# Kernel tuning notes

Measured on AMD Instinct MI355X. Metric: run time of the kernel, lower is better.

The kernel has to match this reference:

```python
import jax, jax.numpy as jnp
import numpy as np

V = 100000   # input_size == output_size (item vocab)
H = 256      # hidden_size
B = 512      # batch_size
L = 1        # num_layers


def setup_inputs() -> dict:
    key = jax.random.key(0)
    k0, k1, k2, k3, k4 = jax.random.split(key, 5)
    s = 1.0 / np.sqrt(H)  # pytorch default uniform bound scale
    return {
        "input": jax.random.randint(k0, (B,), 0, V),
        "target": jax.random.randint(k1, (B,), 0, V),
        "hidden": jnp.zeros((L, B, H), jnp.float32),
        # GRU weights, pytorch gate layout [r; z; n]
        "w_ih": jax.random.uniform(k2, (3 * H, V), jnp.float32, -s, s),
        "w_hh": jax.random.uniform(k3, (3 * H, H), jnp.float32, -s, s),
        "b_ih": jnp.zeros((3 * H,), jnp.float32),
        "b_hh": jnp.zeros((3 * H,), jnp.float32),
        # h2o linear
        "w_out": jax.random.uniform(k4, (V, H), jnp.float32, -s, s),
        "b_out": jnp.zeros((V,), jnp.float32),
    }


def reference(input, target, hidden, w_ih, w_hh, b_ih, b_hh, w_out, b_out):
    # one-hot(input) @ w_ih.T is mathematically a column gather of w_ih
    h = hidden[0]                                        # (B, H)
    gi = jnp.take(w_ih, input, axis=1).T + b_ih          # (B, 3H)
    gh = h @ w_hh.T + b_hh                               # (B, 3H)
    i_r, i_z, i_n = jnp.split(gi, 3, axis=1)
    h_r, h_z, h_n = jnp.split(gh, 3, axis=1)
    r = jax.nn.sigmoid(i_r + h_r)
    z = jax.nn.sigmoid(i_z + h_z)
    n = jnp.tanh(i_n + r * h_n)
    h_new = (1.0 - z) * n + z * h                        # (B, H)
    logit = jnp.tanh(h_new @ w_out.T + b_out)            # (B, V)
    return logit, h_new[None]                            # ((B,V), (L,B,H))
```

## Files before the change

### kernel.cpp

```cpp
#include <hip/hip_runtime.h>
#include <hip/hip_bf16.h>
#include <math.h>

#define V 100000
#define H 256
#define B 512

typedef __bf16 bf16x8 __attribute__((ext_vector_type(8)));
typedef float  f32x4  __attribute__((ext_vector_type(4)));

__device__ __forceinline__ unsigned short f32_bf16_rne(float x) {
    unsigned u = __float_as_uint(x);
    u += 0x7FFFu + ((u >> 16) & 1u);
    return (unsigned short)(u >> 16);
}
__device__ __forceinline__ float bf16u_f32(unsigned short h) {
    return __uint_as_float(((unsigned)h) << 16);
}

__global__ __launch_bounds__(256) void gru_cell_kernel(
    const int*   __restrict__ input,
    const float* __restrict__ hidden,
    const float* __restrict__ w_ih,
    const float* __restrict__ w_hh,
    const float* __restrict__ b_ih,
    const float* __restrict__ b_hh,
    float*       __restrict__ h_out)
{
    const int b = blockIdx.x;
    const int j = threadIdx.x;

    __shared__ float hs[H];
    hs[j] = hidden[b * H + j];
    __syncthreads();

    const int idx = input[b];
    float gi_r = w_ih[ j          * V + idx] + b_ih[j];
    float gi_z = w_ih[(j +     H) * V + idx] + b_ih[j + H];
    float gi_n = w_ih[(j + 2 * H) * V + idx] + b_ih[j + 2 * H];

    const float4* wr = reinterpret_cast<const float4*>(&w_hh[ j          * H]);
    const float4* wz = reinterpret_cast<const float4*>(&w_hh[(j +     H) * H]);
    const float4* wn = reinterpret_cast<const float4*>(&w_hh[(j + 2 * H) * H]);
    const float4* h4 = reinterpret_cast<const float4*>(hs);

    float ar = 0.f, az = 0.f, an = 0.f;
    #pragma unroll 8
    for (int k = 0; k < H / 4; ++k) {
        const float4 hv = h4[k];
        const float4 a  = wr[k];
        const float4 c  = wz[k];
        const float4 d  = wn[k];
        ar += a.x * hv.x + a.y * hv.y + a.z * hv.z + a.w * hv.w;
        az += c.x * hv.x + c.y * hv.y + c.z * hv.z + c.w * hv.w;
        an += d.x * hv.x + d.y * hv.y + d.z * hv.z + d.w * hv.w;
    }

    const float h_r = ar + b_hh[j];
    const float h_z = az + b_hh[j + H];
    const float h_n = an + b_hh[j + 2 * H];

    const float r = 1.f / (1.f + expf(-(gi_r + h_r)));
    const float z = 1.f / (1.f + expf(-(gi_z + h_z)));
    const float n = tanhf(gi_n + r * h_n);
    const float hprev = hs[j];

    h_out[b * H + j] = (1.f - z) * n + z * hprev;
}

#define BM  64
#define BN  128
#define BK  64
#define NVB 782
#define NBB 8

__global__ __launch_bounds__(256) void out_gemm_mfma(
    const float* __restrict__ hnew,
    const float* __restrict__ w_out,
    const float* __restrict__ b_out,
    float*       __restrict__ logit)
{
    __shared__ unsigned short w_hi[BN * BK];
    __shared__ unsigned short w_lo[BN * BK];
    __shared__ unsigned short h_hi[BM * BK];
    __shared__ unsigned short h_lo[BM * BK];

    const int tid  = threadIdx.x;
    const int lane = tid & 63;
    const int wid  = tid >> 6;
    const int wm   = wid >> 1;
    const int wn   = wid & 1;

    const int bid = blockIdx.x;
    const int wg  = (bid & 7) * NVB + (bid >> 3);
    const int bx  = wg & 7;
    const int by  = wg >> 3;
    const int b0  = bx * BM;
    const int v0  = by * BN;

    float4 wreg[8];
    float4 hreg[4];

    auto load_chunk = [&](int k0) {
        #pragma unroll
        for (int i = 0; i < 8; ++i) {
            const int idx4 = i * 256 + tid;
            const int row  = idx4 >> 4;
            const int k4   = (idx4 & 15) << 2;
            int vg = v0 + row; if (vg > V - 1) vg = V - 1;
            wreg[i] = *reinterpret_cast<const float4*>(&w_out[(size_t)vg * H + k0 + k4]);
        }
        #pragma unroll
        for (int i = 0; i < 4; ++i) {
            const int idx4 = i * 256 + tid;
            const int row  = idx4 >> 4;
            const int k4   = (idx4 & 15) << 2;
            hreg[i] = *reinterpret_cast<const float4*>(&hnew[(b0 + row) * H + k0 + k4]);
        }
    };

    auto store_chunk = [&]() {
        #pragma unroll
        for (int i = 0; i < 8; ++i) {
            const int idx4 = i * 256 + tid;
            const int row  = idx4 >> 4;
            const int k4   = (idx4 & 15) << 2;
            const int off  = row * (BK * 2) + ((k4 * 2) ^ ((row & 7) << 4));
            const float f[4] = {wreg[i].x, wreg[i].y, wreg[i].z, wreg[i].w};
            unsigned short hv[4], lv[4];
            #pragma unroll
            for (int j = 0; j < 4; ++j) {
                hv[j] = f32_bf16_rne(f[j]);
                lv[j] = f32_bf16_rne(f[j] - bf16u_f32(hv[j]));
            }
            *reinterpret_cast<ushort4*>(reinterpret_cast<char*>(w_hi) + off) =
                make_ushort4(hv[0], hv[1], hv[2], hv[3]);
            *reinterpret_cast<ushort4*>(reinterpret_cast<char*>(w_lo) + off) =
                make_ushort4(lv[0], lv[1], lv[2], lv[3]);
        }
        #pragma unroll
        for (int i = 0; i < 4; ++i) {
            const int idx4 = i * 256 + tid;
            const int row  = idx4 >> 4;
            const int k4   = (idx4 & 15) << 2;
            const int off  = row * (BK * 2) + ((k4 * 2) ^ ((row & 7) << 4));
            const float f[4] = {hreg[i].x, hreg[i].y, hreg[i].z, hreg[i].w};
            unsigned short hv[4], lv[4];
            #pragma unroll
            for (int j = 0; j < 4; ++j) {
                hv[j] = f32_bf16_rne(f[j]);
                lv[j] = f32_bf16_rne(f[j] - bf16u_f32(hv[j]));
            }
            *reinterpret_cast<ushort4*>(reinterpret_cast<char*>(h_hi) + off) =
                make_ushort4(hv[0], hv[1], hv[2], hv[3]);
            *reinterpret_cast<ushort4*>(reinterpret_cast<char*>(h_lo) + off) =
                make_ushort4(lv[0], lv[1], lv[2], lv[3]);
        }
    };

    f32x4 acc[2][4];
    #pragma unroll
    for (int i = 0; i < 2; ++i)
        #pragma unroll
        for (int n = 0; n < 4; ++n)
            acc[i][n] = f32x4{0.f, 0.f, 0.f, 0.f};

    auto compute = [&]() {
        #pragma unroll
        for (int ks = 0; ks < 2; ++ks) {
            const int kb = ks * 64 + (lane >> 4) * 16;
            bf16x8 ah[2], al[2];
            #pragma unroll
            for (int i = 0; i < 2; ++i) {
                const int row = wm * 32 + i * 16 + (lane & 15);
                const int off = row * (BK * 2) + (kb ^ ((row & 7) << 4));
                ah[i] = *reinterpret_cast<const bf16x8*>(
                            reinterpret_cast<const char*>(h_hi) + off);
                al[i] = *reinterpret_cast<const bf16x8*>(
                            reinterpret_cast<const char*>(h_lo) + off);
            }
            #pragma unroll
            for (int n = 0; n < 4; ++n) {
                const int row = wn * 64 + n * 16 + (lane & 15);
                const int off = row * (BK * 2) + (kb ^ ((row & 7) << 4));
                const bf16x8 bh = *reinterpret_cast<const bf16x8*>(
                            reinterpret_cast<const char*>(w_hi) + off);
                const bf16x8 bl = *reinterpret_cast<const bf16x8*>(
                            reinterpret_cast<const char*>(w_lo) + off);
                #pragma unroll
                for (int i = 0; i < 2; ++i) {
                    acc[i][n] = __builtin_amdgcn_mfma_f32_16x16x32_bf16(ah[i], bh, acc[i][n], 0, 0, 0);
                    acc[i][n] = __builtin_amdgcn_mfma_f32_16x16x32_bf16(ah[i], bl, acc[i][n], 0, 0, 0);
                    acc[i][n] = __builtin_amdgcn_mfma_f32_16x16x32_bf16(al[i], bh, acc[i][n], 0, 0, 0);
                }
            }
        }
    };

    load_chunk(0);
    store_chunk();
    __syncthreads();
    for (int t = 0; t < 4; ++t) {
        if (t < 3) load_chunk((t + 1) * BK);
        compute();
        __syncthreads();
        if (t < 3) { store_chunk(); __syncthreads(); }
    }

    float bias[4];
    int   cols[4];
    #pragma unroll
    for (int n = 0; n < 4; ++n) {
        const int c = v0 + wn * 64 + n * 16 + (lane & 15);
        cols[n] = c;
        bias[n] = (c < V) ? b_out[c] : 0.f;
    }
    const int rbase = b0 + wm * 32 + (lane >> 4) * 4;
    #pragma unroll
    for (int i = 0; i < 2; ++i) {
        #pragma unroll
        for (int r = 0; r < 4; ++r) {
            const int row = rbase + i * 16 + r;
            float* dst = logit + (size_t)row * V;
            #pragma unroll
            for (int n = 0; n < 4; ++n) {
                if (cols[n] < V)
                    dst[cols[n]] = tanhf(acc[i][n][r] + bias[n]);
            }
        }
    }
}

extern "C" void kernel_launch(void* const* d_in, const int* in_sizes, int n_in,
                              void* d_out, int out_size, void* d_ws, size_t ws_size,
                              hipStream_t stream) {
    const int*   input  = (const int*)  d_in[0];
    const float* hidden = (const float*)d_in[2];
    const float* w_ih   = (const float*)d_in[3];
    const float* w_hh   = (const float*)d_in[4];
    const float* b_ih   = (const float*)d_in[5];
    const float* b_hh   = (const float*)d_in[6];
    const float* w_out  = (const float*)d_in[7];
    const float* b_out  = (const float*)d_in[8];

    float* out   = (float*)d_out;
    float* logit = out;
    float* h_new = out + (size_t)B * V;

    gru_cell_kernel<<<B, 256, 0, stream>>>(input, hidden, w_ih, w_hh,
                                           b_ih, b_hh, h_new);

    out_gemm_mfma<<<NVB * NBB, 256, 0, stream>>>(h_new, w_out, b_out, logit);
}
```

Baseline: 230.1 us.

## Pre-split weights to bf16 hi/lo in workspace and stream via direct global-to-LDS loads

Adds a pre-pass that splits w_out into bf16 hi/lo halves in workspace, and has the GRU cell also emit hi/lo halves of h_new. A new GEMM kernel loads these pre-split tiles straight into swizzled LDS with global_load_lds and uses a fast exp2/rcp tanh in the epilogue. The aim is to drop the per-block fp32-to-bf16 split work and register staging in the GEMM. In exchange it adds an extra full pass over w_out each call, reading 100 MB and writing 100 MB. The old path is kept as a fallback when the workspace is too small.

Measured after the change: 253.4 us. +10.1%, slower.

```diff
diff --git a/kernel.cpp b/kernel.cpp
--- a/kernel.cpp
+++ b/kernel.cpp
@@ -16,6 +16,38 @@
 }
 __device__ __forceinline__ float bf16u_f32(unsigned short h) {
     return __uint_as_float(((unsigned)h) << 16);
+}
+__device__ __forceinline__ float fast_tanh(float x) {
+    float e = __builtin_exp2f(x * 2.8853900817779268f);
+    return 1.f - 2.f * __builtin_amdgcn_rcpf(e + 1.f);
+}
+
+#define GLOAD_LDS16(g, l)                                                     \
+    __builtin_amdgcn_global_load_lds(                                         \
+        (const __attribute__((address_space(1))) void*)(g),                   \
+        (__attribute__((address_space(3))) void*)(l), 16, 0, 0)
+
+__global__ __launch_bounds__(256) void split_w_kernel(
+    const float*    __restrict__ w,
+    unsigned short* __restrict__ hi,
+    unsigned short* __restrict__ lo)
+{
+    const int total4 = (V * H) / 4;
+    for (int i = blockIdx.x * blockDim.x + threadIdx.x; i < total4;
+         i += gridDim.x * blockDim.x) {
+        const float4 x = reinterpret_cast<const float4*>(w)[i];
+        const float f[4] = {x.x, x.y, x.z, x.w};
+        ushort4 hv, lv;
+        unsigned short* hp = &hv.x;
+        unsigned short* lp = &lv.x;
+        #pragma unroll
+        for (int j = 0; j < 4; ++j) {
+            hp[j] = f32_bf16_rne(f[j]);
+            lp[j] = f32_bf16_rne(f[j] - bf16u_f32(hp[j]));
+        }
+        reinterpret_cast<ushort4*>(hi)[i] = hv;
+        reinterpret_cast<ushort4*>(lo)[i] = lv;
+    }
 }
 
 __global__ __launch_bounds__(256) void gru_cell_kernel(
@@ -25,7 +57,9 @@
     const float* __restrict__ w_hh,
     const float* __restrict__ b_ih,
     const float* __restrict__ b_hh,
-    float*       __restrict__ h_out)
+    float*       __restrict__ h_out,
+    unsigned short* __restrict__ h_hi_p,
+    unsigned short* __restrict__ h_lo_p)
 {
     const int b = blockIdx.x;
     const int j = threadIdx.x;
@@ -65,7 +99,13 @@
     const float n = tanhf(gi_n + r * h_n);
     const float hprev = hs[j];
 
-    h_out[b * H + j] = (1.f - z) * n + z * hprev;
+    const float val = (1.f - z) * n + z * hprev;
+    h_out[b * H + j] = val;
+    if (h_hi_p != nullptr) {
+        const unsigned short hh = f32_bf16_rne(val);
+        h_hi_p[b * H + j] = hh;
+        h_lo_p[b * H + j] = f32_bf16_rne(val - bf16u_f32(hh));
+    }
 }
 
 #define BM  64
@@ -74,7 +114,130 @@
 #define NVB 782
 #define NBB 8
 
-__global__ __launch_bounds__(256) void out_gemm_mfma(
+__global__ __launch_bounds__(256) void out_gemm_lds(
+    const unsigned short* __restrict__ whi_g,
+    const unsigned short* __restrict__ wlo_g,
+    const unsigned short* __restrict__ hhi_g,
+    const unsigned short* __restrict__ hlo_g,
+    const float*          __restrict__ b_out,
+    float*                __restrict__ logit)
+{
+    __shared__ unsigned short w_hi_s[BN * BK];
+    __shared__ unsigned short w_lo_s[BN * BK];
+    __shared__ unsigned short h_hi_s[BM * BK];
+    __shared__ unsigned short h_lo_s[BM * BK];
+
+    const int tid  = threadIdx.x;
+    const int lane = tid & 63;
+    const int wid  = tid >> 6;
+    const int wm   = wid >> 1;
+    const int wn   = wid & 1;
+
+    const int bid = blockIdx.x;
+    const int wg  = (bid & 7) * NVB + (bid >> 3);
+    const int bx  = wg & 7;
+    const int by  = wg >> 3;
+    const int b0  = bx * BM;
+    const int v0  = by * BN;
+
+    auto stage = [&](int k0) {
+        #pragma unroll
+        for (int i = 0; i < 4; ++i) {
+            const int p    = i * 4096 + (wid << 10) + (lane << 4);
+            const int row  = p >> 7;
+            const int lb   = p & 127;
+            const int swz  = lb ^ ((row & 7) << 4);
+            int vg = v0 + row; if (vg > V - 1) vg = V - 1;
+            const size_t gb = (size_t)vg * (H * 2) + (size_t)(k0 * 2) + swz;
+            const int dst  = i * 4096 + (wid << 10);
+            GLOAD_LDS16((const char*)whi_g + gb, (char*)w_hi_s + dst);
+            GLOAD_LDS16((const char*)wlo_g + gb, (char*)w_lo_s + dst);
+        }
+        #pragma unroll
+        for (int i = 0; i < 2; ++i) {
+            const int p    = i * 4096 + (wid << 10) + (lane << 4);
+            const int row  = p >> 7;
+            const int lb   = p & 127;
+            const int swz  = lb ^ ((row & 7) << 4);
+            const size_t gb = (size_t)(b0 + row) * (H * 2) + (size_t)(k0 * 2) + swz;
+            const int dst  = i * 4096 + (wid << 10);
+            GLOAD_LDS16((const char*)hhi_g + gb, (char*)h_hi_s + dst);
+            GLOAD_LDS16((const char*)hlo_g + gb, (char*)h_lo_s + dst);
+        }
+    };
+
+    f32x4 acc[2][4];
+    #pragma unroll
+    for (int i = 0; i < 2; ++i)
+        #pragma unroll
+        for (int n = 0; n < 4; ++n)
+            acc[i][n] = f32x4{0.f, 0.f, 0.f, 0.f};
+
+    auto compute = [&]() {
+        #pragma unroll
+        for (int ks = 0; ks < 2; ++ks) {
+            const int kb = ks * 64 + (lane >> 4) * 16;
+            bf16x8 ah[2], al[2];
+            #pragma unroll
+            for (int i = 0; i < 2; ++i) {
+                const int row = wm * 32 + i * 16 + (lane & 15);
+                const int off = row * (BK * 2) + (kb ^ ((row & 7) << 4));
+                ah[i] = *reinterpret_cast<const bf16x8*>(
+                            reinterpret_cast<const char*>(h_hi_s) + off);
+                al[i] = *reinterpret_cast<const bf16x8*>(
+                            reinterpret_cast<const char*>(h_lo_s) + off);
+            }
+            #pragma unroll
+            for (int n = 0; n < 4; ++n) {
+                const int row = wn * 64 + n * 16 + (lane & 15);
+                const int off = row * (BK * 2) + (kb ^ ((row & 7) << 4));
+                const bf16x8 bh = *reinterpret_cast<const bf16x8*>(
+                            reinterpret_cast<const char*>(w_hi_s) + off);
+                const bf16x8 bl = *reinterpret_cast<const bf16x8*>(
+                            reinterpret_cast<const char*>(w_lo_s) + off);
+                #pragma unroll
+                for (int i = 0; i < 2; ++i) {
+                    acc[i][n] = __builtin_amdgcn_mfma_f32_16x16x32_bf16(ah[i], bh, acc[i][n], 0, 0, 0);
+                    acc[i][n] = __builtin_amdgcn_mfma_f32_16x16x32_bf16(ah[i], bl, acc[i][n], 0, 0, 0);
+                    acc[i][n] = __builtin_amdgcn_mfma_f32_16x16x32_bf16(al[i], bh, acc[i][n], 0, 0, 0);
+                }
+            }
+        }
+    };
+
+    #pragma unroll
+    for (int t = 0; t < 4; ++t) {
+        stage(t * BK);
+        __syncthreads();
+        compute();
+        __syncthreads();
+    }
+
+    float bias[4];
+    int   cols[4];
+    #pragma unroll
+    for (int n = 0; n < 4; ++n) {
+        const int c = v0 + wn * 64 + n * 16 + (lane & 15);
+        cols[n] = c;
+        bias[n] = (c < V) ? b_out[c] : 0.f;
+    }
+    const int rbase = b0 + wm * 32 + (lane >> 4) * 4;
+    #pragma unroll
+    for (int i = 0; i < 2; ++i) {
+        #pragma unroll
+        for (int r = 0; r < 4; ++r) {
+            const int row = rbase + i * 16 + r;
+            float* dst = logit + (size_t)row * V;
+            #pragma unroll
+            for (int n = 0; n < 4; ++n) {
+                if (cols[n] < V)
+                    dst[cols[n]] = fast_tanh(acc[i][n][r] + bias[n]);
+            }
+        }
+    }
+}
+
+__global__ __launch_bounds__(256) void out_gemm_mfma_reg(
     const float* __restrict__ hnew,
     const float* __restrict__ w_out,
     const float* __restrict__ b_out,
@@ -247,8 +410,26 @@
     float* logit = out;
     float* h_new = out + (size_t)B * V;
 
-    gru_cell_kernel<<<B, 256, 0, stream>>>(input, hidden, w_ih, w_hh,
-                                           b_ih, b_hh, h_new);
-
-    out_gemm_mfma<<<NVB * NBB, 256, 0, stream>>>(h_new, w_out, b_out, logit);
-}
+    const size_t nw = (size_t)V * H;
+    const size_t nh = (size_t)B * H;
+    const size_t needed = (2 * nw + 2 * nh) * sizeof(unsigned short);
+
+    if (ws_size >= needed) {
+        unsigned short* whi = (unsigned short*)d_ws;
+        unsigned short* wlo = whi + nw;
+        unsigned short* hhi = wlo + nw;
+        unsigned short* hlo = hhi + nh;
+
+        split_w_kernel<<<2048, 256, 0, stream>>>(w_out, whi, wlo);
+        gru_cell_kernel<<<B, 256, 0, stream>>>(input, hidden, w_ih, w_hh,
+                                               b_ih, b_hh, h_new, hhi, hlo);
+        out_gemm_lds<<<NVB * NBB, 256, 0, stream>>>(whi, wlo, hhi, hlo,
+                                                    b_out, logit);
+    } else {
+        gru_cell_kernel<<<B, 256, 0, stream>>>(input, hidden, w_ih, w_hh,
+                                               b_ih, b_hh, h_new,
+                                               nullptr, nullptr);
+        out_gemm_mfma_reg<<<NVB * NBB, 256, 0, stream>>>(h_new, w_out,
+                                                         b_out, logit);
+    }
+}
```
